# Kernel optimization log

Measured on AMD Instinct MI355X. Metric: run time of the kernel, lower is better.

## Reference

```python
import jax, jax.numpy as jnp
import numpy as np

B, T, D = 2, 4096, 1024
HQ, HKV, HD = 16, 4, 64   # 16 query heads, 4 KV heads (kv_groups=4), head_dim=64
WIN = 256                 # sliding window radius (left == right == 256)


def setup_inputs() -> dict:
    key = jax.random.key(0)
    ks = jax.random.split(key, 9)
    s = 0.02  # small init scale for stable softmax logits
    return {
        "x": jax.random.normal(ks[0], (B, T, D), jnp.float32),
        "wq": jax.random.normal(ks[1], (D, HQ * HD), jnp.float32) * s,
        "bq": jnp.zeros((HQ * HD,), jnp.float32),
        "wk": jax.random.normal(ks[2], (D, HKV * HD), jnp.float32) * s,
        "bk": jnp.zeros((HKV * HD,), jnp.float32),
        "wv": jax.random.normal(ks[3], (D, HKV * HD), jnp.float32) * s,
        "bv": jnp.zeros((HKV * HD,), jnp.float32),
        "wo": jax.random.normal(ks[4], (HQ * HD, D), jnp.float32) * s,
        "bo": jnp.zeros((D,), jnp.float32),
    }


def _banded_gqa(q, k, v, left, right):
    """Sliding-window GQA attention: query i attends keys in [i-left, i+right].
    Never materializes the full [B,H,T,T] score matrix; uses banded blocks."""
    Bq, Tq, Hq, d = q.shape
    Hkv = k.shape[2]
    G = Hq // Hkv                      # query heads per KV head
    bs = max(left, right)              # block size == window radius; T % bs == 0
    nb = Tq // bs
    # queries: [B, nb, bs, Hkv, G, d]
    qb = q.reshape(Bq, nb, bs, Hkv, G, d)
    # gather 3 neighboring key/value blocks per query block (pad one block each side)
    pad = ((0, 0), (bs, bs), (0, 0), (0, 0))
    idx = jnp.arange(nb)[:, None] * bs + jnp.arange(3 * bs)[None, :]  # into padded seq
    kctx = jnp.pad(k, pad)[:, idx]     # [B, nb, 3bs, Hkv, d]
    vctx = jnp.pad(v, pad)[:, idx]     # [B, nb, 3bs, Hkv, d]
    scale = 1.0 / jnp.sqrt(jnp.asarray(d, q.dtype))
    # banded scores: [B, nb, Hkv, G, bs, 3bs]
    scores = jnp.einsum('bnqhgd,bnkhd->bnhgqk', qb, kctx) * scale
    qpos = jnp.arange(nb)[:, None, None] * bs + jnp.arange(bs)[None, :, None]
    kpos = (jnp.arange(nb)[:, None, None] - 1) * bs + jnp.arange(3 * bs)[None, None, :]
    valid = (kpos >= 0) & (kpos < Tq) & (kpos >= qpos - left) & (kpos <= qpos + right)
    scores = jnp.where(valid[None, :, None, None, :, :], scores, jnp.asarray(-1e30, scores.dtype))
    p = jax.nn.softmax(scores, axis=-1)
    out = jnp.einsum('bnhgqk,bnkhd->bnqhgd', p, vctx)
    return out.reshape(Bq, Tq, Hq, d)


def reference(x, wq, bq, wk, bk, wv, bv, wo, bo):
    q = (x @ wq + bq).reshape(B, T, HQ, HD)
    k = (x @ wk + bk).reshape(B, T, HKV, HD)
    v = (x @ wv + bv).reshape(B, T, HKV, HD)
    y = _banded_gqa(q, k, v, WIN, WIN)       # [B, T, HQ, HD]
    y = y.reshape(B, T, HQ * HD)
    return y @ wo + bo                        # dropout=0.0, deterministic -> identity
```

## Files before the change

kernel.cpp:

```cpp
#include <hip/hip_runtime.h>

typedef unsigned short u16;
typedef u16 u16x4 __attribute__((ext_vector_type(4)));
typedef u16 u16x8 __attribute__((ext_vector_type(8)));
typedef __bf16 bf16x8 __attribute__((ext_vector_type(8)));
typedef float f32x4 __attribute__((ext_vector_type(4)));

#define DEVINL static __device__ __forceinline__

DEVINL u16 f2bf(float f) {
    unsigned u = __builtin_bit_cast(unsigned, f);
    u += 0x7fff + ((u >> 16) & 1);
    return (u16)(u >> 16);
}

DEVINL u16 pbf(float f) {
    unsigned u = __builtin_bit_cast(unsigned, f);
    return (u16)((u + 0x8000) >> 16);
}

DEVINL f32x4 mfma_bf16(u16x8 a, u16x8 b, f32x4 c) {
    return __builtin_amdgcn_mfma_f32_16x16x32_bf16(
        __builtin_bit_cast(bf16x8, a), __builtin_bit_cast(bf16x8, b), c, 0, 0, 0);
}

DEVINL void gload16(const void* g, void* lds) {
    __builtin_amdgcn_global_load_lds(
        (const __attribute__((address_space(1))) void*)g,
        (__attribute__((address_space(3))) void*)lds, 16, 0, 0);
}


__global__ void cvt_x_kernel(const float4* __restrict__ x4, u16x4* __restrict__ o4) {
    int idx = blockIdx.x * 256 + threadIdx.x;
    float4 a = x4[idx];
    u16x4 o;
    o[0] = f2bf(a.x); o[1] = f2bf(a.y); o[2] = f2bf(a.z); o[3] = f2bf(a.w);
    o4[idx] = o;
}

__global__ void fill_bias(const float* __restrict__ bq, const float* __restrict__ bk,
                          const float* __restrict__ bv, float* __restrict__ dst) {
    int i = blockIdx.x * 256 + threadIdx.x;
    if (i < 1024) dst[i] = bq[i];
    else if (i < 1280) dst[i] = bk[i - 1024];
    else if (i < 1536) dst[i] = bv[i - 1280];
}

__global__ void twt_kernel(const float* __restrict__ src, u16* __restrict__ dst,
                           int N, int rowOff) {
    __shared__ float t[64][65];
    int k0 = blockIdx.x * 64, n0 = blockIdx.y * 64;
    int tid = threadIdx.x;
#pragma unroll
    for (int j = 0; j < 16; j++) {
        int idx = j * 256 + tid; int r = idx >> 6, c = idx & 63;
        t[r][c] = src[(size_t)(k0 + r) * N + n0 + c];
    }
    __syncthreads();
#pragma unroll
    for (int j = 0; j < 16; j++) {
        int idx = j * 256 + tid; int r = idx >> 6, c = idx & 63;
        dst[(size_t)(rowOff + n0 + r) * 1024 + k0 + c] = f2bf(t[c][r]);
    }
}

__global__ void tv_kernel(const u16* __restrict__ qkv, u16* __restrict__ vt) {
    __shared__ u16 t[64][68];
    int t0 = blockIdx.x * 64; int h = blockIdx.y; int b = blockIdx.z;
    int tid = threadIdx.x;
#pragma unroll
    for (int j = 0; j < 16; j++) {
        int idx = j * 256 + tid; int r = idx >> 6, c = idx & 63;
        t[r][c] = qkv[(size_t)(b * 4096 + t0 + r) * 1536 + 1280 + h * 64 + c];
    }
    __syncthreads();
#pragma unroll
    for (int j = 0; j < 16; j++) {
        int idx = j * 256 + tid; int r = idx >> 6, c = idx & 63;
        vt[(size_t)((b * 4 + h) * 64 + r) * 4096 + t0 + c] = t[c][r];
    }
}


template <bool F32OUT>
__global__ __launch_bounds__(256, 2) void gemm_bt(
    const u16* __restrict__ A, const u16* __restrict__ Bt, void* __restrict__ Cp,
    const float* __restrict__ bias, int M, int N, int K, int qn, float qscale) {
    __shared__ __align__(16) u16 As[128 * 64];
    __shared__ __align__(16) u16 Bs[128 * 64];
    int tid = threadIdx.x; int l = tid & 63; int w = tid >> 6;

    int nwg = gridDim.x * gridDim.y;
    int lin = blockIdx.y * gridDim.x + blockIdx.x;
    int q_ = nwg >> 3, r_ = nwg & 7;
    int xcd = lin & 7, i_ = lin >> 3;
    int wgid = (xcd < r_ ? xcd * (q_ + 1) : r_ * (q_ + 1) + (xcd - r_) * q_) + i_;
    int m0 = (wgid / gridDim.x) * 128, n0 = (wgid % gridDim.x) * 128;

    int wm = (w >> 1) * 64, wn = (w & 1) * 64;
    f32x4 acc[4][4] = {};

    int srow[4], scol[4];
#pragma unroll
    for (int c = 0; c < 4; c++) {
        int b = (w * 4 + c) * 1024 + l * 16;
        int row = b >> 7, inner = b & 127;
        srow[c] = row;
        scol[c] = (inner ^ ((row & 7) << 4)) >> 1;
    }
    int nk = K >> 6;
    for (int kt = 0; kt < nk; ++kt) {
        int kb = kt << 6;
#pragma unroll
        for (int c = 0; c < 4; c++) {
            gload16(A + (size_t)(m0 + srow[c]) * K + kb + scol[c], (char*)As + (w * 4 + c) * 1024);
            gload16(Bt + (size_t)(n0 + srow[c]) * K + kb + scol[c], (char*)Bs + (w * 4 + c) * 1024);
        }
        __syncthreads();
#pragma unroll
        for (int kc = 0; kc < 2; ++kc) {
            int co = (kc * 32 + (l >> 4) * 8) * 2;
            u16x8 af[4], bf[4];
#pragma unroll
            for (int mf = 0; mf < 4; ++mf) {
                int row = wm + mf * 16 + (l & 15);
                af[mf] = *(const u16x8*)((const char*)As + row * 128 + (co ^ ((row & 7) << 4)));
            }
#pragma unroll
            for (int nf = 0; nf < 4; ++nf) {
                int row = wn + nf * 16 + (l & 15);
                bf[nf] = *(const u16x8*)((const char*)Bs + row * 128 + (co ^ ((row & 7) << 4)));
            }
#pragma unroll
            for (int mf = 0; mf < 4; ++mf)
#pragma unroll
                for (int nf = 0; nf < 4; ++nf)
                    acc[mf][nf] = mfma_bf16(af[mf], bf[nf], acc[mf][nf]);
        }
        __syncthreads();
    }
#pragma unroll
    for (int mf = 0; mf < 4; ++mf) {
#pragma unroll
        for (int nf = 0; nf < 4; ++nf) {
            int col = n0 + wn + nf * 16 + (l & 15);
            float bv = bias ? bias[col] : 0.0f;
            float scl = (col < qn) ? qscale : 1.0f;
#pragma unroll
            for (int r = 0; r < 4; r++) {
                int row = m0 + wm + mf * 16 + (l >> 4) * 4 + r;
                float v = (acc[mf][nf][r] + bv) * scl;
                if (F32OUT) ((float*)Cp)[(size_t)row * N + col] = v;
                else        ((u16*)Cp)[(size_t)row * N + col] = f2bf(v);
            }
        }
    }
}


__global__ __launch_bounds__(512, 8) void attn_kernel(
    const u16* __restrict__ qkv, const u16* __restrict__ vt, u16* __restrict__ y) {
    __shared__ __align__(16) u16 Ks[64 * 64];
    __shared__ __align__(16) u16 Vs[64 * 64];
    __shared__ __align__(16) u16 Ps[8][16 * 64];
    int tid = threadIdx.x, l = tid & 63, w = tid >> 6;
    int qb = ((blockIdx.x & 7) << 3) | (blockIdx.x >> 3);
    int h = blockIdx.y >> 1, hp = blockIdx.y & 1, b = blockIdx.z;
    int qstart = qb * 64;
    size_t rowbase = (size_t)b * 4096;
    int hq = h * 4 + hp * 2 + (w >> 2);
    int qrow0 = (w & 3) * 16;

    u16x8 qf_[2];
#pragma unroll
    for (int kc = 0; kc < 2; ++kc)
        qf_[kc] = *(const u16x8*)(qkv + (rowbase + qstart + qrow0 + (l & 15)) * 1536
                                  + hq * 64 + kc * 32 + (l >> 4) * 8);

    f32x4 o[4] = {};
    float mrow = -__builtin_inff(), srow_ = 0.f;

    const u16* kbase_ptr = qkv + 1024 + h * 64;
    const u16* vbase_ptr = vt + (size_t)((b * 4 + h) * 64) * 4096;

    int sb_ = w * 1024 + l * 16;
    int g_row = sb_ >> 7, g_inner = sb_ & 127;
    int g_col = (g_inner ^ ((g_row & 7) << 4)) >> 1;

#pragma unroll
    for (int kstart = qstart - 256; kstart <= qstart + 256; kstart += 64) {
        if (kstart < 0 || kstart >= 4096) continue;
        gload16(kbase_ptr + (rowbase + kstart + g_row) * 1536 + g_col, (char*)Ks + w * 1024);
        gload16(vbase_ptr + (size_t)g_row * 4096 + kstart + g_col, (char*)Vs + w * 1024);
        __syncthreads();

        f32x4 st[4] = {};
#pragma unroll
        for (int kc = 0; kc < 2; ++kc) {
            int co = (kc * 32 + (l >> 4) * 8) * 2;
#pragma unroll
            for (int kf = 0; kf < 4; ++kf) {
                int row = kf * 16 + (l & 15);
                u16x8 kfr = *(const u16x8*)((const char*)Ks + row * 128 + (co ^ ((row & 7) << 4)));
                st[kf] = mfma_bf16(kfr, qf_[kc], st[kf]);
            }
        }

        bool mlo = (kstart == qstart - 256);
        bool mhi = (kstart == qstart + 256);

        int qoff = qrow0 + (l & 15);
        float pmax = -1e30f;
        float sv[4][4];
#pragma unroll
        for (int kf = 0; kf < 4; ++kf)
#pragma unroll
            for (int r = 0; r < 4; r++) {
                int koff = kf * 16 + (l >> 4) * 4 + r;
                float v = st[kf][r];
                if (mlo && koff < qoff) v = -1e30f;
                if (mhi && koff > qoff) v = -1e30f;
                sv[kf][r] = v;
                pmax = fmaxf(pmax, v);
            }
        pmax = fmaxf(pmax, __shfl_xor(pmax, 16));
        pmax = fmaxf(pmax, __shfl_xor(pmax, 32));

        bool resc = !__all(pmax - mrow <= 8.0f);
        float newm = resc ? fmaxf(mrow, pmax) : mrow;
        float psum = 0.f;
#pragma unroll
        for (int kf = 0; kf < 4; ++kf) {
            u16x4 pk;
#pragma unroll
            for (int r = 0; r < 4; r++) {
                float e = __builtin_amdgcn_exp2f(sv[kf][r] - newm);
                psum += e;
                pk[r] = pbf(e);
            }
            int row = l & 15;
            int keyc = kf * 16 + (l >> 4) * 4;
            *(u16x4*)((char*)Ps[w] + ((row * 128 + keyc * 2) ^ ((row & 7) << 4))) = pk;
        }
        psum += __shfl_xor(psum, 16);
        psum += __shfl_xor(psum, 32);
        if (resc) {
            float fs = __builtin_amdgcn_exp2f(mrow - newm);
            srow_ = srow_ * fs + psum;
            mrow = newm;
#pragma unroll
            for (int r = 0; r < 4; r++) {
                float fb = __shfl(fs, (l >> 4) * 4 + r);
#pragma unroll
                for (int nf = 0; nf < 4; ++nf) o[nf][r] *= fb;
            }
        } else {
            srow_ += psum;
        }

#pragma unroll
        for (int kc = 0; kc < 2; ++kc) {
            int co = (kc * 32 + (l >> 4) * 8) * 2;
            int prow = l & 15;
            u16x8 pa = *(const u16x8*)((const char*)Ps[w] + ((prow * 128 + co) ^ ((prow & 7) << 4)));
#pragma unroll
            for (int nf = 0; nf < 4; ++nf) {
                int row = nf * 16 + (l & 15);
                u16x8 vb = *(const u16x8*)((const char*)Vs + row * 128 + (co ^ ((row & 7) << 4)));
                o[nf] = mfma_bf16(pa, vb, o[nf]);
            }
        }
        __syncthreads();
    }

    float inv = 1.0f / srow_;
#pragma unroll
    for (int r = 0; r < 4; r++) {
        float sb = __shfl(inv, (l >> 4) * 4 + r);
        int row = qstart + qrow0 + (l >> 4) * 4 + r;
#pragma unroll
        for (int nf = 0; nf < 4; ++nf) {
            int col = hq * 64 + nf * 16 + (l & 15);
            y[(rowbase + row) * 1024 + col] = f2bf(o[nf][r] * sb);
        }
    }
}


extern "C" void kernel_launch(void* const* d_in, const int* in_sizes, int n_in,
                              void* d_out, int out_size, void* d_ws, size_t ws_size,
                              hipStream_t stream) {
    const float* x  = (const float*)d_in[0];
    const float* wq = (const float*)d_in[1];
    const float* bq = (const float*)d_in[2];
    const float* wk = (const float*)d_in[3];
    const float* bk = (const float*)d_in[4];
    const float* wv = (const float*)d_in[5];
    const float* bv = (const float*)d_in[6];
    const float* wo = (const float*)d_in[7];
    const float* bo = (const float*)d_in[8];
    float* out = (float*)d_out;

    char* p = (char*)d_ws;
    u16* xb     = (u16*)p;   p += (size_t)8192 * 1024 * 2;
    u16* wqkvt  = (u16*)p;   p += (size_t)1536 * 1024 * 2;
    u16* wot    = (u16*)p;   p += (size_t)1024 * 1024 * 2;
    float* bqkv = (float*)p; p += 8192;
    u16* qkvb   = (u16*)p;   p += (size_t)8192 * 1536 * 2;
    u16* vtb    = (u16*)p;   p += (size_t)512 * 4096 * 2;
    u16* yb     = (u16*)p;

    cvt_x_kernel<<<8192, 256, 0, stream>>>((const float4*)x, (u16x4*)xb);
    fill_bias<<<6, 256, 0, stream>>>(bq, bk, bv, bqkv);
    twt_kernel<<<dim3(16, 16), 256, 0, stream>>>(wq, wqkvt, 1024, 0);
    twt_kernel<<<dim3(16, 4),  256, 0, stream>>>(wk, wqkvt, 256, 1024);
    twt_kernel<<<dim3(16, 4),  256, 0, stream>>>(wv, wqkvt, 256, 1280);
    twt_kernel<<<dim3(16, 16), 256, 0, stream>>>(wo, wot, 1024, 0);

    gemm_bt<false><<<dim3(12, 64), 256, 0, stream>>>(xb, wqkvt, qkvb, bqkv,
                                                     8192, 1536, 1024, 1024, 0.18033688f);
    tv_kernel<<<dim3(64, 4, 2), 256, 0, stream>>>(qkvb, vtb);
    attn_kernel<<<dim3(64, 8, 2), 512, 0, stream>>>(qkvb, vtb, yb);
    gemm_bt<true><<<dim3(8, 64), 256, 0, stream>>>(yb, wot, out, bo,
                                                   8192, 1024, 1024, 0, 1.0f);
}
```

Baseline: 130.3 us.

## Read K/V fragments directly from global memory in attention, drop LDS staging

The attention kernel no longer stages K and V tiles in shared memory with block-wide barriers. Each wave loads its MFMA operand fragments straight from global (L2-cached) memory. Blocks shrink to 256 threads covering one query head, so the grid doubles along the head axis. This removes the LDS traffic and the __syncthreads per key tile, but K/V reuse across the four heads of a group now depends on cache hits. The global loads are strided row reads and may be poorly coalesced.

New measurement: 210.9 us. 1.62x slower.

```diff
diff --git a/kernel.cpp b/kernel.cpp
--- a/kernel.cpp
+++ b/kernel.cpp
@@ -159,18 +159,16 @@
 }
 
 
-__global__ __launch_bounds__(512, 8) void attn_kernel(
+__global__ __launch_bounds__(256, 3) void attn_kernel(
     const u16* __restrict__ qkv, const u16* __restrict__ vt, u16* __restrict__ y) {
-    __shared__ __align__(16) u16 Ks[64 * 64];
-    __shared__ __align__(16) u16 Vs[64 * 64];
-    __shared__ __align__(16) u16 Ps[8][16 * 64];
+    __shared__ __align__(16) u16 Ps[4][16 * 64];
     int tid = threadIdx.x, l = tid & 63, w = tid >> 6;
     int qb = ((blockIdx.x & 7) << 3) | (blockIdx.x >> 3);
-    int h = blockIdx.y >> 1, hp = blockIdx.y & 1, b = blockIdx.z;
+    int hq = blockIdx.y, b = blockIdx.z;
+    int h = hq >> 2;
     int qstart = qb * 64;
     size_t rowbase = (size_t)b * 4096;
-    int hq = h * 4 + hp * 2 + (w >> 2);
-    int qrow0 = (w & 3) * 16;
+    int qrow0 = w * 16;
 
     u16x8 qf_[2];
 #pragma unroll
@@ -184,25 +182,18 @@
     const u16* kbase_ptr = qkv + 1024 + h * 64;
     const u16* vbase_ptr = vt + (size_t)((b * 4 + h) * 64) * 4096;
 
-    int sb_ = w * 1024 + l * 16;
-    int g_row = sb_ >> 7, g_inner = sb_ & 127;
-    int g_col = (g_inner ^ ((g_row & 7) << 4)) >> 1;
-
-#pragma unroll
-    for (int kstart = qstart - 256; kstart <= qstart + 256; kstart += 64) {
-        if (kstart < 0 || kstart >= 4096) continue;
-        gload16(kbase_ptr + (rowbase + kstart + g_row) * 1536 + g_col, (char*)Ks + w * 1024);
-        gload16(vbase_ptr + (size_t)g_row * 4096 + kstart + g_col, (char*)Vs + w * 1024);
-        __syncthreads();
-
+    int klo = qstart - 256; if (klo < 0) klo = 0;
+    int khi = qstart + 256; if (khi > 4096 - 64) khi = 4096 - 64;
+
+    for (int kstart = klo; kstart <= khi; kstart += 64) {
         f32x4 st[4] = {};
 #pragma unroll
         for (int kc = 0; kc < 2; ++kc) {
-            int co = (kc * 32 + (l >> 4) * 8) * 2;
+            const u16* kp = kbase_ptr + (rowbase + kstart + (l & 15)) * 1536
+                            + kc * 32 + (l >> 4) * 8;
 #pragma unroll
             for (int kf = 0; kf < 4; ++kf) {
-                int row = kf * 16 + (l & 15);
-                u16x8 kfr = *(const u16x8*)((const char*)Ks + row * 128 + (co ^ ((row & 7) << 4)));
+                u16x8 kfr = *(const u16x8*)(kp + kf * 16 * 1536);
                 st[kf] = mfma_bf16(kfr, qf_[kc], st[kf]);
             }
         }
@@ -264,14 +255,14 @@
             int co = (kc * 32 + (l >> 4) * 8) * 2;
             int prow = l & 15;
             u16x8 pa = *(const u16x8*)((const char*)Ps[w] + ((prow * 128 + co) ^ ((prow & 7) << 4)));
+            const u16* vp = vbase_ptr + (size_t)(l & 15) * 4096 + kstart
+                            + kc * 32 + (l >> 4) * 8;
 #pragma unroll
             for (int nf = 0; nf < 4; ++nf) {
-                int row = nf * 16 + (l & 15);
-                u16x8 vb = *(const u16x8*)((const char*)Vs + row * 128 + (co ^ ((row & 7) << 4)));
+                u16x8 vb = *(const u16x8*)(vp + (size_t)nf * 16 * 4096);
                 o[nf] = mfma_bf16(pa, vb, o[nf]);
             }
         }
-        __syncthreads();
     }
 
     float inv = 1.0f / srow_;
@@ -321,7 +312,7 @@
     gemm_bt<false><<<dim3(12, 64), 256, 0, stream>>>(xb, wqkvt, qkvb, bqkv,
                                                      8192, 1536, 1024, 1024, 0.18033688f);
     tv_kernel<<<dim3(64, 4, 2), 256, 0, stream>>>(qkvb, vtb);
-    attn_kernel<<<dim3(64, 8, 2), 512, 0, stream>>>(qkvb, vtb, yb);
+    attn_kernel<<<dim3(64, 16, 2), 256, 0, stream>>>(qkvb, vtb, yb);
     gemm_bt<true><<<dim3(8, 64), 256, 0, stream>>>(yb, wot, out, bo,
                                                    8192, 1024, 1024, 0, 1.0f);
 }
```
